# Kernel optimization log

Measured on AMD Instinct MI355X. Metric: run time of the kernel, lower is better.

## Reference

```python
import jax, jax.numpy as jnp
import numpy as np

DIM = 128
GROUPS = [1, 2, 2, 3]


def setup_inputs() -> dict:
    key = jax.random.key(0)
    ks = jax.random.split(key, 8)
    c = DIM
    def p(k, shape, scale=0.02):
        return jax.random.normal(k, shape, dtype=jnp.float32) * scale
    return {
        "x": jax.random.normal(ks[0], (8, c, 128, 128), dtype=jnp.float32),
        "temperature": jnp.ones((4, 1, 1), dtype=jnp.float32),
        "w_qkv": p(ks[1], (3 * c, c)),            # Conv2d(dim, 3*dim, 1), bias=False
        "w_dw": p(ks[2], (3 * c, 1, 3, 3)),        # depthwise 3x3, groups=3*dim
        "w_proj": p(ks[3], (c, c)),                # Conv2d(dim, dim, 1), bias=False
        "w_gate": p(ks[4], (c, c)),                # Intra gatingConv (Conv1d k=1)
        "b_gate": jnp.zeros((c,), jnp.float32),
        "w_down": p(ks[5], (c // 2, c)),           # Intra down
        "b_down": jnp.zeros((c // 2,), jnp.float32),
        "w_up": p(ks[6], (c, c // 2)),             # Intra up
        "b_up": jnp.zeros((c,), jnp.float32),
    }


def _group_sizes(c):
    total = sum(GROUPS)
    sizes = [int(r / total * c) for r in GROUPS]
    sizes[-1] += c - sum(sizes)
    return sizes


def _forward(x, temperature, w_qkv, w_dw, w_proj, w_gate, b_gate,
             w_down, b_down, w_up, b_up):
    b, c, h, w = x.shape
    L = h * w
    # qkv = dwconv3x3(conv1x1(x))
    qkv = jnp.einsum('bchw,oc->bohw', x, w_qkv)
    qkv = jax.lax.conv_general_dilated(
        qkv, w_dw, (1, 1), 'SAME', feature_group_count=3 * c,
        dimension_numbers=('NCHW', 'OIHW', 'NCHW'))
    q, k, v = jnp.split(qkv.reshape(b, 3 * c, L), 3, axis=1)
    # ReGroup: sort channels by mean q activation (descending), split into groups
    channel_mean = q.mean(axis=(0, 2))            # (c,)
    idx = jnp.argsort(-channel_mean)
    q, k, v = q[:, idx], k[:, idx], v[:, idx]
    sizes = _group_sizes(c)
    outs, caches, cache_means = [], [], []
    start = 0
    for i, g in enumerate(sizes):
        qg = q[:, start:start + g]
        kg = k[:, start:start + g]
        vg = v[:, start:start + g]
        start += g
        qn = qg / jnp.maximum(jnp.linalg.norm(qg, axis=-1, keepdims=True), 1e-12)
        kn = kg / jnp.maximum(jnp.linalg.norm(kg, axis=-1, keepdims=True), 1e-12)
        attn = jax.nn.softmax(
            jnp.einsum('bcl,bdl->bcd', qn, kn) * temperature[i, 0, 0], axis=-1)
        outs.append(jnp.einsum('bcd,bdl->bcl', attn, vg))   # (b, g, L)
        tc = jax.lax.stop_gradient(qn + kn)                 # detached cache
        caches.append(tc)
        # per-group mean over L, channel-tiled/padded to c (for cache update)
        gm = tc.mean(axis=-1)                               # (b, g)
        rep = max(1, c // g)
        gm = jnp.tile(gm, (1, rep))
        gm = gm[:, :c] if gm.shape[1] >= c else jnp.pad(gm, ((0, 0), (0, c - gm.shape[1])))
        cache_means.append(gm)
    out_all = jnp.concatenate(outs, axis=1)       # (b, c, L)
    tmp_caches = jnp.concatenate(caches, axis=1)  # (b, c, L)
    # CalculateCurrentLayerCache: bilinear upsample of (1,1) map == broadcast
    s = int(L ** 0.5 + 0.9999)
    acc = sum(cache_means) / float(len(cache_means))        # (b, c)
    qv_cache = jnp.broadcast_to((acc * 0.9)[:, :, None, None], (b, c, s, s))
    # Intra cache modulation: gated = gelu(conv(x1+x2)) * (x1+x2); up(down(gated))
    sxy = out_all + tmp_caches
    gating = jax.nn.gelu(jnp.einsum('bcl,oc->bol', sxy, w_gate) + b_gate[:, None],
                         approximate=False)
    gated = gating * sxy
    mod = jnp.einsum('bcl,oc->bol', gated, w_down) + b_down[:, None]
    mod = jnp.einsum('bcl,oc->bol', mod, w_up) + b_up[:, None]
    out_all = mod + out_all
    out_all = jnp.einsum('bchw,oc->bohw', out_all.reshape(b, c, h, w), w_proj)
    return out_all, qv_cache


def reference(x, temperature, w_qkv, w_dw, w_proj, w_gate, b_gate,
              w_down, b_down, w_up, b_up):
    return _forward(x, temperature, w_qkv, w_dw, w_proj, w_gate, b_gate,
                    w_down, b_down, w_up, b_up)
```

## Files before the change

kernel.cpp:

```cpp
#include <hip/hip_runtime.h>
#include <math.h>

#define B_ 8
#define C_ 128
#define O3_ 384
#define H_ 128
#define W_ 128
#define L_ 16384
#define NS_ 64
#define MAXP_ 2304

typedef float f32x4 __attribute__((ext_vector_type(4)));
typedef short bf16x8 __attribute__((ext_vector_type(8)));

static __device__ __forceinline__ ushort f2bf(float f) {
    uint u = __float_as_uint(f);
    u += 0x7fffu + ((u >> 16) & 1u);
    return (ushort)(u >> 16);
}
static __device__ __forceinline__ float bf2f(ushort h) {
    return __uint_as_float(((uint)h) << 16);
}

__global__ __launch_bounds__(256) void transp_k(const float* __restrict__ x, float* __restrict__ xT)
{
    __shared__ float t[32][33];
    const int b = blockIdx.z;
    const int c0 = blockIdx.y * 32, l0 = blockIdx.x * 32;
    const int tx = threadIdx.x & 31, ty = threadIdx.x >> 5;
#pragma unroll
    for (int i = 0; i < 4; i++) {
        int c = ty + i * 8;
        t[c][tx] = x[((size_t)b * C_ + c0 + c) * L_ + l0 + tx];
    }
    __syncthreads();
#pragma unroll
    for (int i = 0; i < 4; i++) {
        int l = ty + i * 8;
        xT[((size_t)b * L_ + l0 + l) * C_ + c0 + tx] = t[tx][l];
    }
}

template<int KD, int OT, int MODE>
__global__ __launch_bounds__(256) void mgemm_k(
    const float* __restrict__ Wt, const float* __restrict__ bias,
    const float* __restrict__ Xa, const float* __restrict__ E0,
    float* __restrict__ Y)
{
    constexpr int NR = OT / 32;
    __shared__ short sAh[128][40];
    __shared__ short sAl[128][40];
    __shared__ short sBh[OT][40];
    __shared__ short sBl[OT][40];
    const int tid = threadIdx.x;
    const int lane = tid & 63;
    const int wid = tid >> 6;
    const int wr = wid >> 1, wc = wid & 1;
    const int lB = blockIdx.x * 128;
    const int oB = blockIdx.y * OT;
    const int ON = gridDim.y * OT;
    const int b = blockIdx.z;
    const int ln15 = lane & 15, lg = lane >> 4;

    f32x4 acc[4][NR];
#pragma unroll
    for (int m = 0; m < 4; m++)
#pragma unroll
        for (int n = 0; n < NR; n++)
#pragma unroll
            for (int r = 0; r < 4; r++) acc[m][n][r] = 0.f;

    for (int kc = 0; kc < KD; kc += 32) {
#pragma unroll
        for (int p = 0; p < 4; p++) {
            int f4 = tid + p * 256;
            int l = f4 >> 3, c4 = f4 & 7;
            float4 v = *reinterpret_cast<const float4*>(
                &Xa[((size_t)b * L_ + lB + l) * KD + kc + c4 * 4]);
            ushort h0 = f2bf(v.x), h1 = f2bf(v.y), h2 = f2bf(v.z), h3 = f2bf(v.w);
            ushort g0 = f2bf(v.x - bf2f(h0)), g1 = f2bf(v.y - bf2f(h1));
            ushort g2 = f2bf(v.z - bf2f(h2)), g3 = f2bf(v.w - bf2f(h3));
            uint* ah = reinterpret_cast<uint*>(&sAh[l][0]);
            uint* al = reinterpret_cast<uint*>(&sAl[l][0]);
            ah[c4 * 2 + 0] = (uint)h0 | ((uint)h1 << 16);
            ah[c4 * 2 + 1] = (uint)h2 | ((uint)h3 << 16);
            al[c4 * 2 + 0] = (uint)g0 | ((uint)g1 << 16);
            al[c4 * 2 + 1] = (uint)g2 | ((uint)g3 << 16);
        }
#pragma unroll
        for (int p = 0; p < OT / 32; p++) {
            int f4 = tid + p * 256;
            int o = f4 >> 3, c4 = f4 & 7;
            float4 v = *reinterpret_cast<const float4*>(
                &Wt[(size_t)(oB + o) * KD + kc + c4 * 4]);
            ushort h0 = f2bf(v.x), h1 = f2bf(v.y), h2 = f2bf(v.z), h3 = f2bf(v.w);
            ushort g0 = f2bf(v.x - bf2f(h0)), g1 = f2bf(v.y - bf2f(h1));
            ushort g2 = f2bf(v.z - bf2f(h2)), g3 = f2bf(v.w - bf2f(h3));
            uint* bh = reinterpret_cast<uint*>(&sBh[o][0]);
            uint* bl = reinterpret_cast<uint*>(&sBl[o][0]);
            bh[c4 * 2 + 0] = (uint)h0 | ((uint)h1 << 16);
            bh[c4 * 2 + 1] = (uint)h2 | ((uint)h3 << 16);
            bl[c4 * 2 + 0] = (uint)g0 | ((uint)g1 << 16);
            bl[c4 * 2 + 1] = (uint)g2 | ((uint)g3 << 16);
        }
        __syncthreads();
        bf16x8 Ah[4], Al[4], Bh[NR], Bl[NR];
#pragma unroll
        for (int m = 0; m < 4; m++) {
            int row = wr * 64 + m * 16 + ln15;
            Ah[m] = *reinterpret_cast<const bf16x8*>(&sAh[row][lg * 8]);
            Al[m] = *reinterpret_cast<const bf16x8*>(&sAl[row][lg * 8]);
        }
#pragma unroll
        for (int n = 0; n < NR; n++) {
            int row = wc * (OT / 2) + n * 16 + ln15;
            Bh[n] = *reinterpret_cast<const bf16x8*>(&sBh[row][lg * 8]);
            Bl[n] = *reinterpret_cast<const bf16x8*>(&sBl[row][lg * 8]);
        }
#pragma unroll
        for (int m = 0; m < 4; m++)
#pragma unroll
            for (int n = 0; n < NR; n++) {
                acc[m][n] = __builtin_amdgcn_mfma_f32_16x16x32_bf16(Ah[m], Bh[n], acc[m][n], 0, 0, 0);
                acc[m][n] = __builtin_amdgcn_mfma_f32_16x16x32_bf16(Ah[m], Bl[n], acc[m][n], 0, 0, 0);
                acc[m][n] = __builtin_amdgcn_mfma_f32_16x16x32_bf16(Al[m], Bh[n], acc[m][n], 0, 0, 0);
            }
        __syncthreads();
    }

#pragma unroll
    for (int m = 0; m < 4; m++) {
        const int lg4 = lB + wr * 64 + m * 16 + lg * 4;
#pragma unroll
        for (int n = 0; n < NR; n++) {
            const int o = oB + wc * (OT / 2) + n * 16 + ln15;
            if constexpr (MODE == 4) {
                float4 r4 = {acc[m][n][0], acc[m][n][1], acc[m][n][2], acc[m][n][3]};
                *reinterpret_cast<float4*>(&Y[((size_t)b * ON + o) * L_ + lg4]) = r4;
            } else {
                float bv = (MODE != 0) ? bias[o] : 0.f;
#pragma unroll
                for (int r = 0; r < 4; r++) {
                    size_t yi = ((size_t)b * L_ + lg4 + r) * ON + o;
                    float a = acc[m][n][r] + bv;
                    if constexpr (MODE == 1)
                        a = 0.5f * a * (1.f + erff(a * 0.70710678118654752f)) * E0[yi];
                    if constexpr (MODE == 3) a += E0[yi];
                    Y[yi] = a;
                }
            }
        }
    }
}

__global__ __launch_bounds__(256) void dwconv_k(const float* __restrict__ in,
    const float* __restrict__ wdw, float* __restrict__ outp)
{
    __shared__ float tile[10][130];
    const int ch = blockIdx.y, b = blockIdx.z;
    const int y0 = blockIdx.x * 8;
    const int tid = threadIdx.x;
    const size_t base = ((size_t)b * O3_ + ch) * L_;
    for (int id = tid; id < 1300; id += 256) {
        int r = id / 130, cc = id - r * 130;
        int gy = y0 - 1 + r, gx = cc - 1;
        float v = 0.f;
        if (gy >= 0 && gy < H_ && gx >= 0 && gx < W_) v = in[base + (size_t)gy * W_ + gx];
        tile[r][cc] = v;
    }
    __syncthreads();
    const float* wp = wdw + ch * 9;
    const float w0 = wp[0], w1 = wp[1], w2 = wp[2], w3 = wp[3], w4 = wp[4],
                w5 = wp[5], w6 = wp[6], w7 = wp[7], w8 = wp[8];
    const int tx = tid & 127, ty0 = tid >> 7;
#pragma unroll
    for (int rr = 0; rr < 4; rr++) {
        int r = ty0 + rr * 2;
        float s =
            tile[r + 0][tx + 0] * w0 + tile[r + 0][tx + 1] * w1 + tile[r + 0][tx + 2] * w2 +
            tile[r + 1][tx + 0] * w3 + tile[r + 1][tx + 1] * w4 + tile[r + 1][tx + 2] * w5 +
            tile[r + 2][tx + 0] * w6 + tile[r + 2][tx + 1] * w7 + tile[r + 2][tx + 2] * w8;
        outp[base + (size_t)(y0 + r) * W_ + tx] = s;
    }
}

__global__ __launch_bounds__(256) void sums_k(const float* __restrict__ dw,
    float* __restrict__ sumq, float* __restrict__ sumk,
    float* __restrict__ ssq, float* __restrict__ ssk)
{
    const int c = blockIdx.x, b = blockIdx.y, tid = threadIdx.x;
    const float4* qr = reinterpret_cast<const float4*>(dw + ((size_t)b * O3_ + c) * L_);
    const float4* kr = reinterpret_cast<const float4*>(dw + ((size_t)b * O3_ + 128 + c) * L_);
    float sq = 0.f, s2q = 0.f, sk = 0.f, s2k = 0.f;
    for (int i = tid; i < L_ / 4; i += 256) {
        float4 q4 = qr[i], k4 = kr[i];
        sq += (q4.x + q4.y) + (q4.z + q4.w);
        sk += (k4.x + k4.y) + (k4.z + k4.w);
        s2q += q4.x * q4.x + q4.y * q4.y + q4.z * q4.z + q4.w * q4.w;
        s2k += k4.x * k4.x + k4.y * k4.y + k4.z * k4.z + k4.w * k4.w;
    }
    __shared__ float sm[4][256];
    sm[0][tid] = sq; sm[1][tid] = sk; sm[2][tid] = s2q; sm[3][tid] = s2k;
    __syncthreads();
    for (int st = 128; st > 0; st >>= 1) {
        if (tid < st) {
            sm[0][tid] += sm[0][tid + st]; sm[1][tid] += sm[1][tid + st];
            sm[2][tid] += sm[2][tid + st]; sm[3][tid] += sm[3][tid + st];
        }
        __syncthreads();
    }
    if (tid == 0) {
        sumq[b * 128 + c] = sm[0][0]; sumk[b * 128 + c] = sm[1][0];
        ssq[b * 128 + c]  = sm[2][0]; ssk[b * 128 + c]  = sm[3][0];
    }
}

__global__ void combine_k(const float* __restrict__ sumq, const float* __restrict__ sumk,
    const float* __restrict__ ssq, const float* __restrict__ ssk,
    int* __restrict__ idxp, float* __restrict__ rqc, float* __restrict__ rkc,
    float* __restrict__ gm)
{
    const int t = threadIdx.x;
    __shared__ double cms[128];
    double s = 0.0;
    for (int b = 0; b < B_; b++) s += (double)sumq[b * 128 + t];
    cms[t] = s;
    float rqv[B_], rkv[B_];
    for (int b = 0; b < B_; b++) {
        rqv[b] = 1.f / fmaxf(sqrtf(ssq[b * 128 + t]), 1e-12f);
        rkv[b] = 1.f / fmaxf(sqrtf(ssk[b * 128 + t]), 1e-12f);
        rqc[b * 128 + t] = rqv[b];
        rkc[b * 128 + t] = rkv[b];
    }
    __syncthreads();
    const double mv = cms[t];
    int r = 0;
    for (int j = 0; j < 128; j++) {
        double o = cms[j];
        if (o > mv || (o == mv && j < t)) r++;
    }
    idxp[r] = t;
    for (int b = 0; b < B_; b++)
        gm[b * 128 + r] = (rqv[b] * sumq[b * 128 + t] + rkv[b] * sumk[b * 128 + t]) * (1.0f / L_);
}

template<int G>
__global__ __launch_bounds__(256) void score_k(const float* __restrict__ dw, const int* __restrict__ idxp,
    int start, int gi, float* __restrict__ spart)
{
    constexpr int TS = G / 16;
    const int split = blockIdx.x, b = blockIdx.y;
    const int tid = threadIdx.x, tx = tid & 15, ty = tid >> 4;
    __shared__ float sQ[G][66];
    __shared__ float sK[G][66];
    __shared__ int sc[G];
    if (tid < G) sc[tid] = idxp[start + tid];
    __syncthreads();

    float acc[TS][TS];
#pragma unroll
    for (int i = 0; i < TS; i++)
#pragma unroll
        for (int j = 0; j < TS; j++) acc[i][j] = 0.f;

    const int l0 = split * (L_ / NS_);
    constexpr int LPT = (G * 64) / 256;
    for (int chk = 0; chk < L_ / NS_; chk += 64) {
#pragma unroll
        for (int i = 0; i < LPT; i++) {
            int id = tid + i * 256;
            int row = id >> 6, lc = id & 63;
            size_t base = ((size_t)b * O3_ + sc[row]) * L_ + l0 + chk + lc;
            sQ[row][lc] = dw[base];
            sK[row][lc] = dw[base + (size_t)128 * L_];
        }
        __syncthreads();
#pragma unroll
        for (int kk = 0; kk < 64; kk++) {
            float qv[TS], kv[TS];
#pragma unroll
            for (int j = 0; j < TS; j++) { qv[j] = sQ[ty * TS + j][kk]; kv[j] = sK[tx * TS + j][kk]; }
#pragma unroll
            for (int i = 0; i < TS; i++)
#pragma unroll
                for (int j = 0; j < TS; j++)
                    acc[i][j] = fmaf(qv[i], kv[j], acc[i][j]);
        }
        __syncthreads();
    }
    float* op = spart + (((size_t)(b * 4 + gi)) * NS_ + split) * MAXP_;
#pragma unroll
    for (int i = 0; i < TS; i++)
#pragma unroll
        for (int j = 0; j < TS; j++)
            op[(ty * TS + i) * G + tx * TS + j] = acc[i][j];
}

__global__ __launch_bounds__(256) void softmax_k(const float* __restrict__ spart,
    const float* __restrict__ rqc, const float* __restrict__ rkc, const int* __restrict__ idxp,
    const float* __restrict__ temp, float* __restrict__ attn)
{
    const int gi = blockIdx.x, b = blockIdx.y;
    const int g = (gi == 0) ? 16 : (gi == 3 ? 48 : 32);
    const int start = (gi == 0) ? 0 : (gi == 1 ? 16 : (gi == 2 ? 48 : 80));
    __shared__ float S[MAXP_];
    __shared__ int sidx[48];
    if (threadIdx.x < g) sidx[threadIdx.x] = idxp[start + threadIdx.x];
    __syncthreads();
    const float tv = temp[gi];
    for (int p = threadIdx.x; p < g * g; p += 256) {
        float s = 0.f;
        const float* sp = spart + ((size_t)(b * 4 + gi)) * NS_ * MAXP_ + p;
        for (int k = 0; k < NS_; k++) s += sp[(size_t)k * MAXP_];
        int cc = p / g, dd = p - cc * g;
        S[p] = s * rqc[b * 128 + sidx[cc]] * rkc[b * 128 + sidx[dd]] * tv;
    }
    __syncthreads();
    const int wv = threadIdx.x >> 6, lane = threadIdx.x & 63;
    for (int r = wv; r < g; r += 4) {
        float val = (lane < g) ? S[r * g + lane] : -1e30f;
        float mx = val;
        for (int m = 32; m > 0; m >>= 1) mx = fmaxf(mx, __shfl_xor(mx, m));
        float e = (lane < g) ? expf(val - mx) : 0.f;
        float sum = e;
        for (int m = 32; m > 0; m >>= 1) sum += __shfl_xor(sum, m);
        if (lane < g) attn[((size_t)(b * 4 + gi)) * MAXP_ + r * g + lane] = e / sum;
    }
}

template<int G>
__global__ __launch_bounds__(256) void av2_k(const float* __restrict__ dw, const int* __restrict__ idxp,
    const float* __restrict__ rqc, const float* __restrict__ rkc,
    const float* __restrict__ attn, int start, int gi,
    float* __restrict__ outallT, float* __restrict__ sxyT)
{
    constexpr int C4 = G / 4;
    constexpr int GP = G + 1;
    const int b = blockIdx.y;
    const int lB = blockIdx.x * 64;
    const int tid = threadIdx.x;
    __shared__ float sA[G * GP];
    __shared__ float sV[64][GP], sQ[64][GP], sK[64][GP];
    __shared__ int cv[G];
    __shared__ float rqs[G], rks[G];
    if (tid < G) {
        int c0 = idxp[start + tid];
        cv[tid] = c0;
        rqs[tid] = rqc[b * 128 + c0];
        rks[tid] = rkc[b * 128 + c0];
    }
    for (int p = tid; p < G * G; p += 256) {
        int cc = p / G, dd = p - cc * G;
        sA[cc * GP + dd] = attn[((size_t)(b * 4 + gi)) * MAXP_ + p];
    }
    __syncthreads();
    for (int idx = tid; idx < 64 * G; idx += 256) {
        int l = idx & 63, d = idx >> 6;
        size_t base = ((size_t)b * O3_ + cv[d]) * L_ + lB + l;
        sQ[l][d] = dw[base];
        sK[l][d] = dw[base + (size_t)128 * L_];
        sV[l][d] = dw[base + (size_t)256 * L_];
    }
    __syncthreads();
    const int strip = tid & 3, l = tid >> 2;
    float acc[C4];
#pragma unroll
    for (int j = 0; j < C4; j++) acc[j] = 0.f;
    for (int d = 0; d < G; d++) {
        float vd = sV[l][d];
#pragma unroll
        for (int j = 0; j < C4; j++)
            acc[j] = fmaf(sA[(strip * C4 + j) * GP + d], vd, acc[j]);
    }
    const size_t ob = ((size_t)b * L_ + lB + l) * C_ + start + strip * C4;
    float sv[C4];
#pragma unroll
    for (int j = 0; j < C4; j++) {
        int c = strip * C4 + j;
        sv[j] = acc[j] + rqs[c] * sQ[l][c] + rks[c] * sK[l][c];
    }
#pragma unroll
    for (int j = 0; j < C4; j += 4) {
        float4 o4 = {acc[j], acc[j + 1], acc[j + 2], acc[j + 3]};
        float4 s4 = {sv[j], sv[j + 1], sv[j + 2], sv[j + 3]};
        *reinterpret_cast<float4*>(&outallT[ob + j]) = o4;
        *reinterpret_cast<float4*>(&sxyT[ob + j]) = s4;
    }
}

__global__ __launch_bounds__(256) void qvc_k(const float* __restrict__ gm, float* __restrict__ outq)
{
    const int cpos = blockIdx.x, b = blockIdx.y;
    const float* g = gm + b * 128;
    float v = g[cpos & 15] + g[16 + (cpos & 31)] + g[48 + (cpos & 31)];
    if (cpos < 96) v += g[80 + (cpos % 48)];
    v *= 0.225f;
    float4 vv = {v, v, v, v};
    float4* op = reinterpret_cast<float4*>(outq + ((size_t)b * C_ + cpos) * L_);
    for (int i = threadIdx.x; i < L_ / 4; i += 256) op[i] = vv;
}

extern "C" void kernel_launch(void* const* d_in, const int* in_sizes, int n_in,
                              void* d_out, int out_size, void* d_ws, size_t ws_size,
                              hipStream_t stream)
{
    const float* x     = (const float*)d_in[0];
    const float* temp  = (const float*)d_in[1];
    const float* wqkv  = (const float*)d_in[2];
    const float* wdw   = (const float*)d_in[3];
    const float* wproj = (const float*)d_in[4];
    const float* wgate = (const float*)d_in[5];
    const float* bgate = (const float*)d_in[6];
    const float* wdown = (const float*)d_in[7];
    const float* bdown = (const float*)d_in[8];
    const float* wup   = (const float*)d_in[9];
    const float* bup   = (const float*)d_in[10];
    float* out = (float*)d_out;
    float* ws  = (float*)d_ws;

    float* qkvCL  = ws;
    float* xT     = ws + 50331648ull;
    float* dwCL   = ws + 50331648ull;
    float* outallT= ws;
    float* sxyT   = ws + 16777216ull;
    float* gatedT = ws + 33554432ull;
    float* mod1T  = ws + 16777216ull;
    float* out2T  = ws + 25165824ull;

    float* spart = out;
    float* attn  = out + 4718592ull;
    float* sumq  = out + 4800000ull;
    float* sumk  = out + 4801024ull;
    float* ssq   = out + 4802048ull;
    float* ssk   = out + 4803072ull;
    float* rqc   = out + 4804096ull;
    float* rkc   = out + 4805120ull;
    float* gm    = out + 4806144ull;
    int*   idxp  = (int*)(out + 4807168ull);

    transp_k<<<dim3(512, 4, 8), 256, 0, stream>>>(x, xT);
    mgemm_k<128, 128, 4><<<dim3(128, 3, 8), 256, 0, stream>>>(wqkv, nullptr, xT, nullptr, qkvCL);
    dwconv_k<<<dim3(16, 384, 8), 256, 0, stream>>>(qkvCL, wdw, dwCL);
    sums_k<<<dim3(128, 8), 256, 0, stream>>>(dwCL, sumq, sumk, ssq, ssk);
    combine_k<<<1, 128, 0, stream>>>(sumq, sumk, ssq, ssk, idxp, rqc, rkc, gm);
    score_k<16><<<dim3(NS_, 8), 256, 0, stream>>>(dwCL, idxp, 0, 0, spart);
    score_k<32><<<dim3(NS_, 8), 256, 0, stream>>>(dwCL, idxp, 16, 1, spart);
    score_k<32><<<dim3(NS_, 8), 256, 0, stream>>>(dwCL, idxp, 48, 2, spart);
    score_k<48><<<dim3(NS_, 8), 256, 0, stream>>>(dwCL, idxp, 80, 3, spart);
    softmax_k<<<dim3(4, 8), 256, 0, stream>>>(spart, rqc, rkc, idxp, temp, attn);
    av2_k<16><<<dim3(256, 8), 256, 0, stream>>>(dwCL, idxp, rqc, rkc, attn, 0, 0, outallT, sxyT);
    av2_k<32><<<dim3(256, 8), 256, 0, stream>>>(dwCL, idxp, rqc, rkc, attn, 16, 1, outallT, sxyT);
    av2_k<32><<<dim3(256, 8), 256, 0, stream>>>(dwCL, idxp, rqc, rkc, attn, 48, 2, outallT, sxyT);
    av2_k<48><<<dim3(256, 8), 256, 0, stream>>>(dwCL, idxp, rqc, rkc, attn, 80, 3, outallT, sxyT);
    mgemm_k<128, 128, 1><<<dim3(128, 1, 8), 256, 0, stream>>>(wgate, bgate, sxyT, sxyT, gatedT);
    qvc_k<<<dim3(128, 8), 256, 0, stream>>>(gm, out + 16777216ull);
    mgemm_k<128, 64, 2><<<dim3(128, 1, 8), 256, 0, stream>>>(wdown, bdown, gatedT, nullptr, mod1T);
    mgemm_k<64, 128, 3><<<dim3(128, 1, 8), 256, 0, stream>>>(wup, bup, mod1T, outallT, out2T);
    mgemm_k<128, 128, 4><<<dim3(128, 1, 8), 256, 0, stream>>>(wproj, nullptr, out2T, nullptr, out);
}
```

Baseline: 710.0 us.

## Store intermediates as bf16 hi/lo pairs, fuse dwconv with stats, merge group kernels

Activations passed between GEMMs are now stored pre-split into bf16 hi and lo halves, so each GEMM loads them directly instead of converting fp32 in every block. The transpose is widened and emits the split form. The depthwise conv is rewritten as a register-sliding row stencil that also computes the per-channel sums, which removes the separate sums kernel. The four score and four AV launches each become one launch indexed by blockIdx.z. The grid order of the GEMMs and their B-fragment loop order also change. Storing intermediates as bf16 pairs keeps near-fp32 precision but adds a rounding step at every stage.

```diff
diff --git a/kernel.cpp b/kernel.cpp
--- a/kernel.cpp
+++ b/kernel.cpp
@@ -22,30 +22,53 @@
     return __uint_as_float(((uint)h) << 16);
 }
 
-__global__ __launch_bounds__(256) void transp_k(const float* __restrict__ x, float* __restrict__ xT)
-{
-    __shared__ float t[32][33];
-    const int b = blockIdx.z;
-    const int c0 = blockIdx.y * 32, l0 = blockIdx.x * 32;
-    const int tx = threadIdx.x & 31, ty = threadIdx.x >> 5;
-#pragma unroll
-    for (int i = 0; i < 4; i++) {
-        int c = ty + i * 8;
-        t[c][tx] = x[((size_t)b * C_ + c0 + c) * L_ + l0 + tx];
-    }
-    __syncthreads();
-#pragma unroll
-    for (int i = 0; i < 4; i++) {
-        int l = ty + i * 8;
-        xT[((size_t)b * L_ + l0 + l) * C_ + c0 + tx] = t[tx][l];
+__global__ __launch_bounds__(256) void transp_k(const float* __restrict__ x,
+    short* __restrict__ xhi, short* __restrict__ xlo)
+{
+    __shared__ float t[128][33];
+    const int b = blockIdx.y;
+    const int l0 = blockIdx.x * 32;
+    const int tid = threadIdx.x;
+    {
+        const int c = tid >> 1, half = tid & 1;
+        const float* src = x + ((size_t)b * C_ + c) * L_ + l0 + half * 16;
+#pragma unroll
+        for (int u = 0; u < 4; u++) {
+            float4 v = *reinterpret_cast<const float4*>(src + u * 4);
+            t[c][half * 16 + u * 4 + 0] = v.x;
+            t[c][half * 16 + u * 4 + 1] = v.y;
+            t[c][half * 16 + u * 4 + 2] = v.z;
+            t[c][half * 16 + u * 4 + 3] = v.w;
+        }
+    }
+    __syncthreads();
+    {
+        const int l = tid >> 3, strip = tid & 7;
+        uint hi[8], lo[8];
+#pragma unroll
+        for (int i = 0; i < 8; i++) {
+            float a0 = t[strip * 16 + 2 * i][l], a1 = t[strip * 16 + 2 * i + 1][l];
+            ushort h0 = f2bf(a0), h1 = f2bf(a1);
+            ushort g0 = f2bf(a0 - bf2f(h0)), g1 = f2bf(a1 - bf2f(h1));
+            hi[i] = (uint)h0 | ((uint)h1 << 16);
+            lo[i] = (uint)g0 | ((uint)g1 << 16);
+        }
+        size_t ob = ((size_t)b * L_ + l0 + l) * C_ + strip * 16;
+        uint4* ph = reinterpret_cast<uint4*>(xhi + ob);
+        uint4* pl = reinterpret_cast<uint4*>(xlo + ob);
+        ph[0] = *reinterpret_cast<uint4*>(&hi[0]);
+        ph[1] = *reinterpret_cast<uint4*>(&hi[4]);
+        pl[0] = *reinterpret_cast<uint4*>(&lo[0]);
+        pl[1] = *reinterpret_cast<uint4*>(&lo[4]);
     }
 }
 
 template<int KD, int OT, int MODE>
 __global__ __launch_bounds__(256) void mgemm_k(
-    const float* __restrict__ Wt, const float* __restrict__ bias,
-    const float* __restrict__ Xa, const float* __restrict__ E0,
-    float* __restrict__ Y)
+    const float* __restrict__ Wf, const float* __restrict__ bias,
+    const short* __restrict__ Ahi, const short* __restrict__ Alo,
+    const float* __restrict__ E0,
+    float* __restrict__ Yf, short* __restrict__ Yhi, short* __restrict__ Ylo)
 {
     constexpr int NR = OT / 32;
     __shared__ short sAh[128][40];
@@ -56,9 +79,9 @@
     const int lane = tid & 63;
     const int wid = tid >> 6;
     const int wr = wid >> 1, wc = wid & 1;
-    const int lB = blockIdx.x * 128;
-    const int oB = blockIdx.y * OT;
-    const int ON = gridDim.y * OT;
+    const int oB = blockIdx.x * OT;
+    const int lB = blockIdx.y * 128;
+    const int ON = gridDim.x * OT;
     const int b = blockIdx.z;
     const int ln15 = lane & 15, lg = lane >> 4;
 
@@ -71,40 +94,25 @@
             for (int r = 0; r < 4; r++) acc[m][n][r] = 0.f;
 
     for (int kc = 0; kc < KD; kc += 32) {
-#pragma unroll
-        for (int p = 0; p < 4; p++) {
-            int f4 = tid + p * 256;
-            int l = f4 >> 3, c4 = f4 & 7;
-            float4 v = *reinterpret_cast<const float4*>(
-                &Xa[((size_t)b * L_ + lB + l) * KD + kc + c4 * 4]);
+        for (int p = tid; p < 512; p += 256) {
+            int l = p >> 2, c8 = (p & 3) * 8;
+            size_t g = ((size_t)b * L_ + lB + l) * KD + kc + c8;
+            *reinterpret_cast<bf16x8*>(&sAh[l][c8]) = *reinterpret_cast<const bf16x8*>(&Ahi[g]);
+            *reinterpret_cast<bf16x8*>(&sAl[l][c8]) = *reinterpret_cast<const bf16x8*>(&Alo[g]);
+        }
+        for (int p = tid; p < OT * 8; p += 256) {
+            int o = p >> 3, c4 = (p & 7) * 4;
+            float4 v = *reinterpret_cast<const float4*>(&Wf[(size_t)(oB + o) * KD + kc + c4]);
             ushort h0 = f2bf(v.x), h1 = f2bf(v.y), h2 = f2bf(v.z), h3 = f2bf(v.w);
             ushort g0 = f2bf(v.x - bf2f(h0)), g1 = f2bf(v.y - bf2f(h1));
             ushort g2 = f2bf(v.z - bf2f(h2)), g3 = f2bf(v.w - bf2f(h3));
-            uint* ah = reinterpret_cast<uint*>(&sAh[l][0]);
-            uint* al = reinterpret_cast<uint*>(&sAl[l][0]);
-            ah[c4 * 2 + 0] = (uint)h0 | ((uint)h1 << 16);
-            ah[c4 * 2 + 1] = (uint)h2 | ((uint)h3 << 16);
-            al[c4 * 2 + 0] = (uint)g0 | ((uint)g1 << 16);
-            al[c4 * 2 + 1] = (uint)g2 | ((uint)g3 << 16);
-        }
-#pragma unroll
-        for (int p = 0; p < OT / 32; p++) {
-            int f4 = tid + p * 256;
-            int o = f4 >> 3, c4 = f4 & 7;
-            float4 v = *reinterpret_cast<const float4*>(
-                &Wt[(size_t)(oB + o) * KD + kc + c4 * 4]);
-            ushort h0 = f2bf(v.x), h1 = f2bf(v.y), h2 = f2bf(v.z), h3 = f2bf(v.w);
-            ushort g0 = f2bf(v.x - bf2f(h0)), g1 = f2bf(v.y - bf2f(h1));
-            ushort g2 = f2bf(v.z - bf2f(h2)), g3 = f2bf(v.w - bf2f(h3));
-            uint* bh = reinterpret_cast<uint*>(&sBh[o][0]);
-            uint* bl = reinterpret_cast<uint*>(&sBl[o][0]);
-            bh[c4 * 2 + 0] = (uint)h0 | ((uint)h1 << 16);
-            bh[c4 * 2 + 1] = (uint)h2 | ((uint)h3 << 16);
-            bl[c4 * 2 + 0] = (uint)g0 | ((uint)g1 << 16);
-            bl[c4 * 2 + 1] = (uint)g2 | ((uint)g3 << 16);
+            uint2 uh = {(uint)h0 | ((uint)h1 << 16), (uint)h2 | ((uint)h3 << 16)};
+            uint2 ul = {(uint)g0 | ((uint)g1 << 16), (uint)g2 | ((uint)g3 << 16)};
+            *reinterpret_cast<uint2*>(&sBh[o][c4]) = uh;
+            *reinterpret_cast<uint2*>(&sBl[o][c4]) = ul;
         }
         __syncthreads();
-        bf16x8 Ah[4], Al[4], Bh[NR], Bl[NR];
+        bf16x8 Ah[4], Al[4];
 #pragma unroll
         for (int m = 0; m < 4; m++) {
             int row = wr * 64 + m * 16 + ln15;
@@ -113,18 +121,16 @@
         }
 #pragma unroll
         for (int n = 0; n < NR; n++) {
-            int row = wc * (OT / 2) + n * 16 + ln15;
-            Bh[n] = *reinterpret_cast<const bf16x8*>(&sBh[row][lg * 8]);
-            Bl[n] = *reinterpret_cast<const bf16x8*>(&sBl[row][lg * 8]);
-        }
-#pragma unroll
-        for (int m = 0; m < 4; m++)
-#pragma unroll
-            for (int n = 0; n < NR; n++) {
-                acc[m][n] = __builtin_amdgcn_mfma_f32_16x16x32_bf16(Ah[m], Bh[n], acc[m][n], 0, 0, 0);
-                acc[m][n] = __builtin_amdgcn_mfma_f32_16x16x32_bf16(Ah[m], Bl[n], acc[m][n], 0, 0, 0);
-                acc[m][n] = __builtin_amdgcn_mfma_f32_16x16x32_bf16(Al[m], Bh[n], acc[m][n], 0, 0, 0);
+            int brow = wc * (OT / 2) + n * 16 + ln15;
+            bf16x8 Bh = *reinterpret_cast<const bf16x8*>(&sBh[brow][lg * 8]);
+            bf16x8 Bl = *reinterpret_cast<const bf16x8*>(&sBl[brow][lg * 8]);
+#pragma unroll
+            for (int m = 0; m < 4; m++) {
+                acc[m][n] = __builtin_amdgcn_mfma_f32_16x16x32_bf16(Ah[m], Bh, acc[m][n], 0, 0, 0);
+                acc[m][n] = __builtin_amdgcn_mfma_f32_16x16x32_bf16(Ah[m], Bl, acc[m][n], 0, 0, 0);
+                acc[m][n] = __builtin_amdgcn_mfma_f32_16x16x32_bf16(Al[m], Bh, acc[m][n], 0, 0, 0);
             }
+        }
         __syncthreads();
     }
 
@@ -136,17 +142,22 @@
             const int o = oB + wc * (OT / 2) + n * 16 + ln15;
             if constexpr (MODE == 4) {
                 float4 r4 = {acc[m][n][0], acc[m][n][1], acc[m][n][2], acc[m][n][3]};
-                *reinterpret_cast<float4*>(&Y[((size_t)b * ON + o) * L_ + lg4]) = r4;
+                *reinterpret_cast<float4*>(&Yf[((size_t)b * ON + o) * L_ + lg4]) = r4;
             } else {
-                float bv = (MODE != 0) ? bias[o] : 0.f;
+                float bv = bias[o];
 #pragma unroll
                 for (int r = 0; r < 4; r++) {
                     size_t yi = ((size_t)b * L_ + lg4 + r) * ON + o;
                     float a = acc[m][n][r] + bv;
-                    if constexpr (MODE == 1)
-                        a = 0.5f * a * (1.f + erff(a * 0.70710678118654752f)) * E0[yi];
+                    if constexpr (MODE == 1) {
+                        float sxy = bf2f((ushort)Ahi[yi]) + bf2f((ushort)Alo[yi]);
+                        a = 0.5f * a * (1.f + erff(a * 0.70710678118654752f)) * sxy;
+                    }
                     if constexpr (MODE == 3) a += E0[yi];
-                    Y[yi] = a;
+                    ushort h = f2bf(a);
+                    ushort g = f2bf(a - bf2f(h));
+                    Yhi[yi] = (short)h;
+                    Ylo[yi] = (short)g;
                 }
             }
         }
@@ -154,64 +165,67 @@
 }
 
 __global__ __launch_bounds__(256) void dwconv_k(const float* __restrict__ in,
-    const float* __restrict__ wdw, float* __restrict__ outp)
-{
-    __shared__ float tile[10][130];
-    const int ch = blockIdx.y, b = blockIdx.z;
-    const int y0 = blockIdx.x * 8;
-    const int tid = threadIdx.x;
-    const size_t base = ((size_t)b * O3_ + ch) * L_;
-    for (int id = tid; id < 1300; id += 256) {
-        int r = id / 130, cc = id - r * 130;
-        int gy = y0 - 1 + r, gx = cc - 1;
-        float v = 0.f;
-        if (gy >= 0 && gy < H_ && gx >= 0 && gx < W_) v = in[base + (size_t)gy * W_ + gx];
-        tile[r][cc] = v;
-    }
-    __syncthreads();
-    const float* wp = wdw + ch * 9;
-    const float w0 = wp[0], w1 = wp[1], w2 = wp[2], w3 = wp[3], w4 = wp[4],
-                w5 = wp[5], w6 = wp[6], w7 = wp[7], w8 = wp[8];
-    const int tx = tid & 127, ty0 = tid >> 7;
-#pragma unroll
-    for (int rr = 0; rr < 4; rr++) {
-        int r = ty0 + rr * 2;
-        float s =
-            tile[r + 0][tx + 0] * w0 + tile[r + 0][tx + 1] * w1 + tile[r + 0][tx + 2] * w2 +
-            tile[r + 1][tx + 0] * w3 + tile[r + 1][tx + 1] * w4 + tile[r + 1][tx + 2] * w5 +
-            tile[r + 2][tx + 0] * w6 + tile[r + 2][tx + 1] * w7 + tile[r + 2][tx + 2] * w8;
-        outp[base + (size_t)(y0 + r) * W_ + tx] = s;
-    }
-}
-
-__global__ __launch_bounds__(256) void sums_k(const float* __restrict__ dw,
+    const float* __restrict__ wdw, float* __restrict__ outp,
     float* __restrict__ sumq, float* __restrict__ sumk,
     float* __restrict__ ssq, float* __restrict__ ssk)
 {
-    const int c = blockIdx.x, b = blockIdx.y, tid = threadIdx.x;
-    const float4* qr = reinterpret_cast<const float4*>(dw + ((size_t)b * O3_ + c) * L_);
-    const float4* kr = reinterpret_cast<const float4*>(dw + ((size_t)b * O3_ + 128 + c) * L_);
-    float sq = 0.f, s2q = 0.f, sk = 0.f, s2k = 0.f;
-    for (int i = tid; i < L_ / 4; i += 256) {
-        float4 q4 = qr[i], k4 = kr[i];
-        sq += (q4.x + q4.y) + (q4.z + q4.w);
-        sk += (k4.x + k4.y) + (k4.z + k4.w);
-        s2q += q4.x * q4.x + q4.y * q4.y + q4.z * q4.z + q4.w * q4.w;
-        s2k += k4.x * k4.x + k4.y * k4.y + k4.z * k4.z + k4.w * k4.w;
-    }
-    __shared__ float sm[4][256];
-    sm[0][tid] = sq; sm[1][tid] = sk; sm[2][tid] = s2q; sm[3][tid] = s2k;
-    __syncthreads();
-    for (int st = 128; st > 0; st >>= 1) {
-        if (tid < st) {
-            sm[0][tid] += sm[0][tid + st]; sm[1][tid] += sm[1][tid + st];
-            sm[2][tid] += sm[2][tid + st]; sm[3][tid] += sm[3][tid + st];
-        }
+    const int ch = blockIdx.x, b = blockIdx.y;
+    const int tid = threadIdx.x;
+    const int tx = tid & 31, band = tid >> 5;
+    const int x0 = tx * 4;
+    const int y0 = band * 16;
+    const size_t base = ((size_t)b * O3_ + ch) * L_;
+    const float* wp = wdw + ch * 9;
+    float w0 = wp[0], w1 = wp[1], w2 = wp[2], w3 = wp[3], w4 = wp[4],
+          w5 = wp[5], w6 = wp[6], w7 = wp[7], w8 = wp[8];
+
+    float s1 = 0.f, s2 = 0.f;
+    float b0[6], b1[6], b2[6];
+
+    auto loadrow = [&](int gy, float* r) {
+        if ((unsigned)gy < (unsigned)H_) {
+            const float* rp = in + base + (size_t)gy * W_;
+            float4 m = *reinterpret_cast<const float4*>(rp + x0);
+            r[0] = (x0 > 0) ? rp[x0 - 1] : 0.f;
+            r[1] = m.x; r[2] = m.y; r[3] = m.z; r[4] = m.w;
+            r[5] = (x0 < W_ - 4) ? rp[x0 + 4] : 0.f;
+        } else {
+            r[0] = r[1] = r[2] = r[3] = r[4] = r[5] = 0.f;
+        }
+    };
+    auto conv3 = [&](const float* ra, const float* rb, const float* rc, int yy) {
+        float o0 = ra[0]*w0 + ra[1]*w1 + ra[2]*w2 + rb[0]*w3 + rb[1]*w4 + rb[2]*w5 + rc[0]*w6 + rc[1]*w7 + rc[2]*w8;
+        float o1 = ra[1]*w0 + ra[2]*w1 + ra[3]*w2 + rb[1]*w3 + rb[2]*w4 + rb[3]*w5 + rc[1]*w6 + rc[2]*w7 + rc[3]*w8;
+        float o2 = ra[2]*w0 + ra[3]*w1 + ra[4]*w2 + rb[2]*w3 + rb[3]*w4 + rb[4]*w5 + rc[2]*w6 + rc[3]*w7 + rc[4]*w8;
+        float o3 = ra[3]*w0 + ra[4]*w1 + ra[5]*w2 + rb[3]*w3 + rb[4]*w4 + rb[5]*w5 + rc[3]*w6 + rc[4]*w7 + rc[5]*w8;
+        float4 o4 = {o0, o1, o2, o3};
+        *reinterpret_cast<float4*>(&outp[base + (size_t)(y0 + yy) * W_ + x0]) = o4;
+        s1 += (o0 + o1) + (o2 + o3);
+        s2 += o0*o0 + o1*o1 + o2*o2 + o3*o3;
+    };
+
+    loadrow(y0 - 1, b0);
+    loadrow(y0,     b1);
+#pragma unroll
+    for (int y3 = 0; y3 < 15; y3 += 3) {
+        loadrow(y0 + y3 + 1, b2); conv3(b0, b1, b2, y3);
+        loadrow(y0 + y3 + 2, b0); conv3(b1, b2, b0, y3 + 1);
+        loadrow(y0 + y3 + 3, b1); conv3(b2, b0, b1, y3 + 2);
+    }
+    loadrow(y0 + 16, b2); conv3(b0, b1, b2, 15);
+
+    __shared__ float r1[256], r2[256];
+    if (ch < 256) {
+        r1[tid] = s1; r2[tid] = s2;
         __syncthreads();
-    }
-    if (tid == 0) {
-        sumq[b * 128 + c] = sm[0][0]; sumk[b * 128 + c] = sm[1][0];
-        ssq[b * 128 + c]  = sm[2][0]; ssk[b * 128 + c]  = sm[3][0];
+        for (int st = 128; st > 0; st >>= 1) {
+            if (tid < st) { r1[tid] += r1[tid + st]; r2[tid] += r2[tid + st]; }
+            __syncthreads();
+        }
+        if (tid == 0) {
+            if (ch < 128) { sumq[b * 128 + ch] = r1[0]; ssq[b * 128 + ch] = r2[0]; }
+            else          { sumk[b * 128 + ch - 128] = r1[0]; ssk[b * 128 + ch - 128] = r2[0]; }
+        }
     }
 }
 
@@ -245,15 +259,13 @@
 }
 
 template<int G>
-__global__ __launch_bounds__(256) void score_k(const float* __restrict__ dw, const int* __restrict__ idxp,
-    int start, int gi, float* __restrict__ spart)
+__device__ __forceinline__ void score_body(const float* __restrict__ dw,
+    const int* __restrict__ idxp, int start, int gi, float* __restrict__ spart,
+    float* sQ, float* sK, int* sc)
 {
     constexpr int TS = G / 16;
     const int split = blockIdx.x, b = blockIdx.y;
     const int tid = threadIdx.x, tx = tid & 15, ty = tid >> 4;
-    __shared__ float sQ[G][66];
-    __shared__ float sK[G][66];
-    __shared__ int sc[G];
     if (tid < G) sc[tid] = idxp[start + tid];
     __syncthreads();
 
@@ -271,15 +283,18 @@
             int id = tid + i * 256;
             int row = id >> 6, lc = id & 63;
             size_t base = ((size_t)b * O3_ + sc[row]) * L_ + l0 + chk + lc;
-            sQ[row][lc] = dw[base];
-            sK[row][lc] = dw[base + (size_t)128 * L_];
+            sQ[row * 66 + lc] = dw[base];
+            sK[row * 66 + lc] = dw[base + (size_t)128 * L_];
         }
         __syncthreads();
 #pragma unroll
         for (int kk = 0; kk < 64; kk++) {
             float qv[TS], kv[TS];
 #pragma unroll
-            for (int j = 0; j < TS; j++) { qv[j] = sQ[ty * TS + j][kk]; kv[j] = sK[tx * TS + j][kk]; }
+            for (int j = 0; j < TS; j++) {
+                qv[j] = sQ[(ty * TS + j) * 66 + kk];
+                kv[j] = sK[(tx * TS + j) * 66 + kk];
+            }
 #pragma unroll
             for (int i = 0; i < TS; i++)
 #pragma unroll
@@ -294,6 +309,20 @@
 #pragma unroll
         for (int j = 0; j < TS; j++)
             op[(ty * TS + i) * G + tx * TS + j] = acc[i][j];
+}
+
+__global__ __launch_bounds__(256) void score_k(const float* __restrict__ dw,
+    const int* __restrict__ idxp, float* __restrict__ spart)
+{
+    __shared__ float sQ[48 * 66];
+    __shared__ float sK[48 * 66];
+    __shared__ int sc[48];
+    switch (blockIdx.z) {
+        case 0: score_body<16>(dw, idxp, 0, 0, spart, sQ, sK, sc); break;
+        case 1: score_body<32>(dw, idxp, 16, 1, spart, sQ, sK, sc); break;
+        case 2: score_body<32>(dw, idxp, 48, 2, spart, sQ, sK, sc); break;
+        default: score_body<48>(dw, idxp, 80, 3, spart, sQ, sK, sc); break;
+    }
 }
 
 __global__ __launch_bounds__(256) void softmax_k(const float* __restrict__ spart,
@@ -329,20 +358,17 @@
 }
 
 template<int G>
-__global__ __launch_bounds__(256) void av2_k(const float* __restrict__ dw, const int* __restrict__ idxp,
-    const float* __restrict__ rqc, const float* __restrict__ rkc,
+__device__ __forceinline__ void av2_body(const float* __restrict__ dw,
+    const int* __restrict__ idxp, const float* __restrict__ rqc, const float* __restrict__ rkc,
     const float* __restrict__ attn, int start, int gi,
-    float* __restrict__ outallT, float* __restrict__ sxyT)
+    float* __restrict__ outallT, short* __restrict__ sxyhi, short* __restrict__ sxylo,
+    float* sA, float* sV, float* sQ2, float* sK2, int* cv, float* rqs, float* rks)
 {
     constexpr int C4 = G / 4;
     constexpr int GP = G + 1;
     const int b = blockIdx.y;
     const int lB = blockIdx.x * 64;
     const int tid = threadIdx.x;
-    __shared__ float sA[G * GP];
-    __shared__ float sV[64][GP], sQ[64][GP], sK[64][GP];
-    __shared__ int cv[G];
-    __shared__ float rqs[G], rks[G];
     if (tid < G) {
         int c0 = idxp[start + tid];
         cv[tid] = c0;
@@ -357,9 +383,9 @@
     for (int idx = tid; idx < 64 * G; idx += 256) {
         int l = idx & 63, d = idx >> 6;
         size_t base = ((size_t)b * O3_ + cv[d]) * L_ + lB + l;
-        sQ[l][d] = dw[base];
-        sK[l][d] = dw[base + (size_t)128 * L_];
-        sV[l][d] = dw[base + (size_t)256 * L_];
+        sQ2[l * GP + d] = dw[base];
+        sK2[l * GP + d] = dw[base + (size_t)128 * L_];
+        sV[l * GP + d]  = dw[base + (size_t)256 * L_];
     }
     __syncthreads();
     const int strip = tid & 3, l = tid >> 2;
@@ -367,7 +393,7 @@
 #pragma unroll
     for (int j = 0; j < C4; j++) acc[j] = 0.f;
     for (int d = 0; d < G; d++) {
-        float vd = sV[l][d];
+        float vd = sV[l * GP + d];
 #pragma unroll
         for (int j = 0; j < C4; j++)
             acc[j] = fmaf(sA[(strip * C4 + j) * GP + d], vd, acc[j]);
@@ -377,14 +403,36 @@
 #pragma unroll
     for (int j = 0; j < C4; j++) {
         int c = strip * C4 + j;
-        sv[j] = acc[j] + rqs[c] * sQ[l][c] + rks[c] * sK[l][c];
+        sv[j] = acc[j] + rqs[c] * sQ2[l * GP + c] + rks[c] * sK2[l * GP + c];
     }
 #pragma unroll
     for (int j = 0; j < C4; j += 4) {
         float4 o4 = {acc[j], acc[j + 1], acc[j + 2], acc[j + 3]};
-        float4 s4 = {sv[j], sv[j + 1], sv[j + 2], sv[j + 3]};
         *reinterpret_cast<float4*>(&outallT[ob + j]) = o4;
-        *reinterpret_cast<float4*>(&sxyT[ob + j]) = s4;
+    }
+#pragma unroll
+    for (int j = 0; j < C4; j += 2) {
+        ushort h0 = f2bf(sv[j]), h1 = f2bf(sv[j + 1]);
+        ushort g0 = f2bf(sv[j] - bf2f(h0)), g1 = f2bf(sv[j + 1] - bf2f(h1));
+        *reinterpret_cast<uint*>(&sxyhi[ob + j]) = (uint)h0 | ((uint)h1 << 16);
+        *reinterpret_cast<uint*>(&sxylo[ob + j]) = (uint)g0 | ((uint)g1 << 16);
+    }
+}
+
+__global__ __launch_bounds__(256) void av2_k(const float* __restrict__ dw,
+    const int* __restrict__ idxp, const float* __restrict__ rqc, const float* __restrict__ rkc,
+    const float* __restrict__ attn, float* __restrict__ outallT,
+    short* __restrict__ sxyhi, short* __restrict__ sxylo)
+{
+    __shared__ float sA[48 * 49];
+    __shared__ float sV[64 * 49], sQ2[64 * 49], sK2[64 * 49];
+    __shared__ int cv[48];
+    __shared__ float rqs[48], rks[48];
+    switch (blockIdx.z) {
+        case 0: av2_body<16>(dw, idxp, rqc, rkc, attn, 0, 0, outallT, sxyhi, sxylo, sA, sV, sQ2, sK2, cv, rqs, rks); break;
+        case 1: av2_body<32>(dw, idxp, rqc, rkc, attn, 16, 1, outallT, sxyhi, sxylo, sA, sV, sQ2, sK2, cv, rqs, rks); break;
+        case 2: av2_body<32>(dw, idxp, rqc, rkc, attn, 48, 2, outallT, sxyhi, sxylo, sA, sV, sQ2, sK2, cv, rqs, rks); break;
+        default: av2_body<48>(dw, idxp, rqc, rkc, attn, 80, 3, outallT, sxyhi, sxylo, sA, sV, sQ2, sK2, cv, rqs, rks); break;
     }
 }
 
@@ -418,14 +466,19 @@
     float* out = (float*)d_out;
     float* ws  = (float*)d_ws;
 
-    float* qkvCL  = ws;
-    float* xT     = ws + 50331648ull;
-    float* dwCL   = ws + 50331648ull;
-    float* outallT= ws;
-    float* sxyT   = ws + 16777216ull;
-    float* gatedT = ws + 33554432ull;
-    float* mod1T  = ws + 16777216ull;
-    float* out2T  = ws + 25165824ull;
+    float* qkvCL = ws;
+    float* dwCL  = ws + 50331648ull;
+    short* xThi  = (short*)(ws + 50331648ull);
+    short* xTlo  = xThi + 16777216ull;
+    float* outallT = ws;
+    short* sxyhi   = (short*)(ws + 16777216ull);
+    short* sxylo   = sxyhi + 16777216ull;
+    short* gatedhi = (short*)(ws + 33554432ull);
+    short* gatedlo = gatedhi + 16777216ull;
+    short* mod1hi  = (short*)(ws + 16777216ull);
+    short* mod1lo  = mod1hi + 8388608ull;
+    short* out2hi  = (short*)(ws + 33554432ull);
+    short* out2lo  = out2hi + 16777216ull;
 
     float* spart = out;
     float* attn  = out + 4718592ull;
@@ -438,23 +491,21 @@
     float* gm    = out + 4806144ull;
     int*   idxp  = (int*)(out + 4807168ull);
 
-    transp_k<<<dim3(512, 4, 8), 256, 0, stream>>>(x, xT);
-    mgemm_k<128, 128, 4><<<dim3(128, 3, 8), 256, 0, stream>>>(wqkv, nullptr, xT, nullptr, qkvCL);
-    dwconv_k<<<dim3(16, 384, 8), 256, 0, stream>>>(qkvCL, wdw, dwCL);
-    sums_k<<<dim3(128, 8), 256, 0, stream>>>(dwCL, sumq, sumk, ssq, ssk);
+    transp_k<<<dim3(512, 8), 256, 0, stream>>>(x, xThi, xTlo);
+    mgemm_k<128, 128, 4><<<dim3(3, 128, 8), 256, 0, stream>>>(
+        wqkv, nullptr, xThi, xTlo, nullptr, qkvCL, nullptr, nullptr);
+    dwconv_k<<<dim3(384, 8), 256, 0, stream>>>(qkvCL, wdw, dwCL, sumq, sumk, ssq, ssk);
     combine_k<<<1, 128, 0, stream>>>(sumq, sumk, ssq, ssk, idxp, rqc, rkc, gm);
-    score_k<16><<<dim3(NS_, 8), 256, 0, stream>>>(dwCL, idxp, 0, 0, spart);
-    score_k<32><<<dim3(NS_, 8), 256, 0, stream>>>(dwCL, idxp, 16, 1, spart);
-    score_k<32><<<dim3(NS_, 8), 256, 0, stream>>>(dwCL, idxp, 48, 2, spart);
-    score_k<48><<<dim3(NS_, 8), 256, 0, stream>>>(dwCL, idxp, 80, 3, spart);
+    score_k<<<dim3(NS_, 8, 4), 256, 0, stream>>>(dwCL, idxp, spart);
     softmax_k<<<dim3(4, 8), 256, 0, stream>>>(spart, rqc, rkc, idxp, temp, attn);
-    av2_k<16><<<dim3(256, 8), 256, 0, stream>>>(dwCL, idxp, rqc, rkc, attn, 0, 0, outallT, sxyT);
-    av2_k<32><<<dim3(256, 8), 256, 0, stream>>>(dwCL, idxp, rqc, rkc, attn, 16, 1, outallT, sxyT);
-    av2_k<32><<<dim3(256, 8), 256, 0, stream>>>(dwCL, idxp, rqc, rkc, attn, 48, 2, outallT, sxyT);
-    av2_k<48><<<dim3(256, 8), 256, 0, stream>>>(dwCL, idxp, rqc, rkc, attn, 80, 3, outallT, sxyT);
-    mgemm_k<128, 128, 1><<<dim3(128, 1, 8), 256, 0, stream>>>(wgate, bgate, sxyT, sxyT, gatedT);
+    av2_k<<<dim3(256, 8, 4), 256, 0, stream>>>(dwCL, idxp, rqc, rkc, attn, outallT, sxyhi, sxylo);
+    mgemm_k<128, 128, 1><<<dim3(1, 128, 8), 256, 0, stream>>>(
+        wgate, bgate, sxyhi, sxylo, nullptr, nullptr, gatedhi, gatedlo);
     qvc_k<<<dim3(128, 8), 256, 0, stream>>>(gm, out + 16777216ull);
-    mgemm_k<128, 64, 2><<<dim3(128, 1, 8), 256, 0, stream>>>(wdown, bdown, gatedT, nullptr, mod1T);
-    mgemm_k<64, 128, 3><<<dim3(128, 1, 8), 256, 0, stream>>>(wup, bup, mod1T, outallT, out2T);
-    mgemm_k<128, 128, 4><<<dim3(128, 1, 8), 256, 0, stream>>>(wproj, nullptr, out2T, nullptr, out);
-}
+    mgemm_k<128, 64, 2><<<dim3(1, 128, 8), 256, 0, stream>>>(
+        wdown, bdown, gatedhi, gatedlo, nullptr, nullptr, mod1hi, mod1lo);
+    mgemm_k<64, 128, 3><<<dim3(1, 128, 8), 256, 0, stream>>>(
+        wup, bup, mod1hi, mod1lo, outallT, nullptr, out2hi, out2lo);
+    mgemm_k<128, 128, 4><<<dim3(1, 128, 8), 256, 0, stream>>>(
+        wproj, nullptr, out2hi, out2lo, nullptr, out, nullptr, nullptr);
+}
```

Measured after the change: 828.6 us. 1.17x slower.
